# Performance work log

Hardware: AMD Instinct MI355X
Metric: run time of the kernel (lower is better)

## Reference

```python
import jax, jax.numpy as jnp
import numpy as np

# layer_sizes[i] = (hidden_dim, branching); 3 tree levels with fan-out 8 -> 512 leaf bins
LAYER_SIZES = [[512, 1], [512, 8], [512, 8], [512, 8]]
IN_DIM = LAYER_SIZES[0][0]
BATCH = 8192


def _nets_per_level():
    ns, n = [], 1
    for i in range(len(LAYER_SIZES) - 1):
        ns.append(n)
        n *= LAYER_SIZES[i + 1][1]
    return ns  # [1, 8, 64]


def setup_inputs() -> dict:
    key = jax.random.key(0)
    ks = jax.random.split(key, 16)
    ns = _nets_per_level()
    d = {"inp": jax.random.normal(ks[0], (BATCH, IN_DIM), jnp.float32)}
    k = 1
    for i, n in enumerate(ns):
        h = LAYER_SIZES[i + 1][0]
        w = LAYER_SIZES[i + 1][1]
        # stacked per-net weights (xavier-ish scale)
        d[f"Wx{i}"] = jax.random.normal(ks[k], (n, IN_DIM, h), jnp.float32) / np.float32(np.sqrt(IN_DIM)); k += 1
        d[f"bx{i}"] = jnp.zeros((n, h), jnp.float32)
        d[f"Wp{i}"] = jax.random.normal(ks[k], (n, h, w), jnp.float32) / np.float32(np.sqrt(h)); k += 1
        d[f"bp{i}"] = jnp.zeros((n, w), jnp.float32)
    d["We"] = jax.random.normal(ks[k], (IN_DIM, 1), jnp.float32) / np.float32(np.sqrt(IN_DIM))
    d["be"] = jnp.zeros((1,), jnp.float32)
    return d


def reference(inp, Wx0, bx0, Wp0, bp0, Wx1, bx1, Wp1, bp1, Wx2, bx2, Wp2, bp2, We, be):
    # event indicator head (blockable=False -> single sigmoid unit)
    got_event = jax.nn.sigmoid(inp @ We + be)  # [B, 1]
    Wxs, bxs = [Wx0, Wx1, Wx2], [bx0, bx1, bx2]
    Wps, bps = [Wp0, Wp1, Wp2], [bp0, bp1, bp2]
    probs_out = []
    parent = None  # flattened parent probs [B, n_i]; child j scales by parent[:, j]
    for i in range(3):
        # all nets at this level read the raw input: batched grouped GEMM
        h = jax.nn.relu(jnp.einsum('bi,nih->bnh', inp, Wxs[i]) + bxs[i])   # [B, n, H]
        p = jax.nn.softmax(jnp.einsum('bnh,nhw->bnw', h, Wps[i]) + bps[i], axis=-1)  # [B, n, w]
        if i == 0:
            p = p * got_event[:, :, None]          # get_event_probs, not blockable
        else:
            p = p * parent[:, :, None]             # gather of parent prob column j%w == flat index j
        parent = p.reshape(p.shape[0], -1)         # [B, n*w]
        probs_out.append(jnp.concatenate([parent, 1.0 - got_event], axis=1))
    return tuple(probs_out)
```

## Files before the change

### kernel.cpp

```cpp
#include <hip/hip_runtime.h>

#define IN_DIM 512
#define NBATCH 8192
#define BM 128
#define BK 32
#define HSTR 136

typedef short s16x8 __attribute__((ext_vector_type(8)));
typedef float f32x4 __attribute__((ext_vector_type(4)));

__device__ __forceinline__ unsigned short f2bf(float f) {
    union { float f; unsigned int u; } c;
    c.f = f;
    unsigned int u = c.u;
    u += 0x7fffu + ((u >> 16) & 1u);
    return (unsigned short)(u >> 16);
}

__device__ __forceinline__ void gload16(const unsigned short* g, unsigned short* l) {
    __builtin_amdgcn_global_load_lds(
        (const __attribute__((address_space(1))) void*)g,
        (__attribute__((address_space(3))) void*)l,
        16, 0, 0);
}


__global__ __launch_bounds__(256)
void conv_inp(const float* __restrict__ in, unsigned short* __restrict__ out) {
    int i = (blockIdx.x * 256 + threadIdx.x) * 8;
    float4 a = *(const float4*)&in[i];
    float4 b = *(const float4*)&in[i + 4];
    union { unsigned short u[8]; s16x8 v; } r;
    r.u[0] = f2bf(a.x); r.u[1] = f2bf(a.y); r.u[2] = f2bf(a.z); r.u[3] = f2bf(a.w);
    r.u[4] = f2bf(b.x); r.u[5] = f2bf(b.y); r.u[6] = f2bf(b.z); r.u[7] = f2bf(b.w);
    *(s16x8*)&out[i] = r.v;
}

__global__ __launch_bounds__(256)
void conv_wxT(const float* __restrict__ Wx, unsigned short* __restrict__ WxT) {
    __shared__ unsigned short T[64][80];
    int j  = blockIdx.y;
    int tr = blockIdx.x >> 3;
    int tc = blockIdx.x & 7;
    const float* src = Wx + (size_t)j * IN_DIM * IN_DIM;
    unsigned short* dst = WxT + (size_t)j * IN_DIM * IN_DIM;
    int tid = threadIdx.x;
    int k  = tid >> 2;
    int c0 = (tid & 3) * 16;
    for (int u = 0; u < 16; u += 4) {
        float4 v = *(const float4*)&src[(size_t)(tr * 64 + k) * IN_DIM + tc * 64 + c0 + u];
        T[c0 + u + 0][k] = f2bf(v.x);
        T[c0 + u + 1][k] = f2bf(v.y);
        T[c0 + u + 2][k] = f2bf(v.z);
        T[c0 + u + 3][k] = f2bf(v.w);
    }
    __syncthreads();
    int c  = tid >> 2;
    int k0 = (tid & 3) * 16;
    for (int u = 0; u < 16; u += 8) {
        s16x8 v = *(const s16x8*)&T[c][k0 + u];
        *(s16x8*)&dst[(size_t)(tc * 64 + c) * IN_DIM + tr * 64 + k0 + u] = v;
    }
}

__global__ __launch_bounds__(256)
void conv_wpT(const float* __restrict__ Wp, unsigned short* __restrict__ WpT) {
    int j = blockIdx.x;
    const float* src = Wp + (size_t)j * IN_DIM * 8;
    unsigned short* dst = WpT + (size_t)j * IN_DIM * 8;
    for (int k = threadIdx.x; k < IN_DIM; k += 256)
        for (int w = 0; w < 8; ++w)
            dst[w * IN_DIM + k] = f2bf(src[k * 8 + w]);
}

__global__ __launch_bounds__(256, 2)
void level_fast(const unsigned short* __restrict__ inpB,
                const unsigned short* __restrict__ WxT,
                const float* __restrict__ bx,
                const unsigned short* __restrict__ WpT,
                const float* __restrict__ bp,
                const float* __restrict__ parent,
                int pstride, int poff, int invert_parent,
                float* __restrict__ outp, int ostride)
{
    __shared__ __align__(16) unsigned short lds[BM * HSTR];

    const int tid  = threadIdx.x;
    const int lane = tid & 63;
    const int wv   = tid >> 6;
    const int j    = blockIdx.y;
    const int rowBase = blockIdx.x * BM;
    const int lr  = lane & 15;
    const int kg8 = (lane >> 4) * 8;
    const int rg  = (lane >> 4) * 4;
    const int wm  = (wv & 1) * 64;
    const int wn  = (wv >> 1) * 64;

    const unsigned short* WxTj = WxT + (size_t)j * IN_DIM * IN_DIM;
    const unsigned short* WpTj = WpT + (size_t)j * IN_DIM * 8;

    const int srow  = wv * 32 + (lane >> 2);
    const int sslot = (lane & 3) * 8;

    f32x4 acc2[2] = {};

    for (int nt = 0; nt < 4; ++nt) {
        f32x4 acc[4][4] = {};
        for (int k0 = 0; k0 < IN_DIM; k0 += BK) {
            __syncthreads();
            {
                const unsigned short* ga = inpB + (size_t)(rowBase + srow) * IN_DIM + k0 + sslot;
                const unsigned short* gb = WxTj + (size_t)(nt * BM + srow) * IN_DIM + k0 + sslot;
                gload16(ga,                &lds[wv * 1024]);
                gload16(ga + 16 * IN_DIM,  &lds[wv * 1024 + 512]);
                gload16(gb,                &lds[4096 + wv * 1024]);
                gload16(gb + 16 * IN_DIM,  &lds[4096 + wv * 1024 + 512]);
            }
            __syncthreads();
            s16x8 af[4], bfr[4];
            for (int mt = 0; mt < 4; ++mt)
                af[mt] = *(const s16x8*)&lds[(wm + mt * 16 + lr) * 32 + kg8];
            for (int nn = 0; nn < 4; ++nn)
                bfr[nn] = *(const s16x8*)&lds[4096 + (wn + nn * 16 + lr) * 32 + kg8];
            for (int mt = 0; mt < 4; ++mt)
                for (int nn = 0; nn < 4; ++nn)
                    acc[mt][nn] = __builtin_amdgcn_mfma_f32_16x16x32_bf16(
                        af[mt], bfr[nn], acc[mt][nn], 0, 0, 0);
        }
        __syncthreads();
        for (int nn = 0; nn < 4; ++nn) {
            int ncol = wn + nn * 16 + lr;
            float bxv = bx[(size_t)j * IN_DIM + nt * BM + ncol];
            for (int mt = 0; mt < 4; ++mt)
                for (int v = 0; v < 4; ++v) {
                    float h = acc[mt][nn][v] + bxv;
                    h = h > 0.f ? h : 0.f;
                    lds[(wm + mt * 16 + rg + v) * HSTR + ncol] = f2bf(h);
                }
        }
        __syncthreads();
        for (int k2 = 0; k2 < 4; ++k2) {
            int jw = lr & 7;
            s16x8 b2 = *(const s16x8*)(WpTj + jw * IN_DIM + nt * BM + k2 * 32 + kg8);
            for (int m2 = 0; m2 < 2; ++m2) {
                s16x8 a2 = *(const s16x8*)&lds[(wv * 32 + m2 * 16 + lr) * HSTR + k2 * 32 + kg8];
                acc2[m2] = __builtin_amdgcn_mfma_f32_16x16x32_bf16(a2, b2, acc2[m2], 0, 0, 0);
            }
        }
    }

    bool valid = lr < 8;
    float bpv = valid ? bp[(size_t)j * 8 + lr] : 0.f;
    for (int m2 = 0; m2 < 2; ++m2) {
        for (int v = 0; v < 4; ++v) {
            float x = acc2[m2][v] + bpv;
            float mx = x;
            for (int d = 1; d < 8; d <<= 1)
                mx = fmaxf(mx, __shfl_xor(mx, d, 64));
            float e = __expf(x - mx);
            float s = e;
            for (int d = 1; d < 8; d <<= 1)
                s += __shfl_xor(s, d, 64);
            float p = e / s;
            int gb = rowBase + wv * 32 + m2 * 16 + rg + v;
            float pv = invert_parent ? (1.f - parent[(size_t)gb * pstride + poff])
                                     : parent[(size_t)gb * pstride + j];
            if (valid)
                outp[(size_t)gb * ostride + j * 8 + lr] = p * pv;
        }
    }
}

__global__ __launch_bounds__(256, 2)
void level_ref(const float* __restrict__ inp,
               const float* __restrict__ Wx,
               const float* __restrict__ bx,
               const float* __restrict__ Wp,
               const float* __restrict__ bp,
               const float* __restrict__ parent,
               int pstride, int poff, int invert_parent,
               float* __restrict__ outp, int ostride)
{
    __shared__ __align__(16) unsigned short Ash[128][40];
    __shared__ __align__(16) unsigned short Bsh[128][40];
    __shared__ __align__(16) unsigned short Hsh[128][HSTR];
    __shared__ __align__(16) unsigned short WpSh[8][IN_DIM];

    const int tid  = threadIdx.x;
    const int lane = tid & 63;
    const int wv   = tid >> 6;
    const int j    = blockIdx.y;
    const int rowBase = blockIdx.x * 128;
    const int lr = lane & 15;
    const int kg = (lane >> 4) * 8;
    const int rg = (lane >> 4) * 4;
    const int wm = (wv & 1) * 64;
    const int wn = (wv >> 1) * 64;

    const float* WxJ = Wx + (size_t)j * IN_DIM * IN_DIM;
    const float* WpJ = Wp + (size_t)j * IN_DIM * 8;

    for (int i = tid; i < IN_DIM * 2; i += 256) {
        int k  = i >> 1;
        int w4 = (i & 1) * 4;
        float4 v = *(const float4*)&WpJ[k * 8 + w4];
        WpSh[w4 + 0][k] = f2bf(v.x);
        WpSh[w4 + 1][k] = f2bf(v.y);
        WpSh[w4 + 2][k] = f2bf(v.z);
        WpSh[w4 + 3][k] = f2bf(v.w);
    }

    f32x4 acc2[2] = {};

    for (int nt = 0; nt < 4; ++nt) {
        f32x4 acc[4][4] = {};
        for (int k0 = 0; k0 < IN_DIM; k0 += 32) {
            __syncthreads();
            {
                int kk4 = (tid & 7) * 4;
                int rb  = tid >> 3;
                for (int it = 0; it < 4; ++it) {
                    int r = rb + it * 32;
                    float4 v = *(const float4*)&inp[(size_t)(rowBase + r) * IN_DIM + k0 + kk4];
                    unsigned short* dst = &Ash[r][kk4];
                    dst[0] = f2bf(v.x); dst[1] = f2bf(v.y);
                    dst[2] = f2bf(v.z); dst[3] = f2bf(v.w);
                }
            }
            {
                int n4 = (tid & 31) * 4;
                int kb = tid >> 5;
                for (int it = 0; it < 4; ++it) {
                    int kk = kb + it * 8;
                    float4 v = *(const float4*)&WxJ[(size_t)(k0 + kk) * IN_DIM + nt * 128 + n4];
                    Bsh[n4 + 0][kk] = f2bf(v.x);
                    Bsh[n4 + 1][kk] = f2bf(v.y);
                    Bsh[n4 + 2][kk] = f2bf(v.z);
                    Bsh[n4 + 3][kk] = f2bf(v.w);
                }
            }
            __syncthreads();
            s16x8 af[4], bfr[4];
            for (int mt = 0; mt < 4; ++mt)
                af[mt] = *(const s16x8*)&Ash[wm + mt * 16 + lr][kg];
            for (int nn = 0; nn < 4; ++nn)
                bfr[nn] = *(const s16x8*)&Bsh[wn + nn * 16 + lr][kg];
            for (int mt = 0; mt < 4; ++mt)
                for (int nn = 0; nn < 4; ++nn)
                    acc[mt][nn] = __builtin_amdgcn_mfma_f32_16x16x32_bf16(
                        af[mt], bfr[nn], acc[mt][nn], 0, 0, 0);
        }
        __syncthreads();
        for (int nn = 0; nn < 4; ++nn) {
            int ncol = wn + nn * 16 + lr;
            float bxv = bx[(size_t)j * IN_DIM + nt * 128 + ncol];
            for (int mt = 0; mt < 4; ++mt)
                for (int v = 0; v < 4; ++v) {
                    float h = acc[mt][nn][v] + bxv;
                    h = h > 0.f ? h : 0.f;
                    Hsh[wm + mt * 16 + rg + v][ncol] = f2bf(h);
                }
        }
        __syncthreads();
        {
            s16x8 zero = {};
            for (int k2 = 0; k2 < 128; k2 += 32) {
                s16x8 b2 = (lr < 8) ? *(const s16x8*)&WpSh[lr][nt * 128 + k2 + kg] : zero;
                for (int m2 = 0; m2 < 2; ++m2) {
                    s16x8 a2 = *(const s16x8*)&Hsh[wv * 32 + m2 * 16 + lr][k2 + kg];
                    acc2[m2] = __builtin_amdgcn_mfma_f32_16x16x32_bf16(a2, b2, acc2[m2], 0, 0, 0);
                }
            }
        }
    }

    bool valid = lr < 8;
    float bpv = valid ? bp[(size_t)j * 8 + lr] : 0.f;
    for (int m2 = 0; m2 < 2; ++m2) {
        for (int v = 0; v < 4; ++v) {
            float x = acc2[m2][v] + bpv;
            float mx = x;
            for (int d = 1; d < 8; d <<= 1)
                mx = fmaxf(mx, __shfl_xor(mx, d, 64));
            float e = __expf(x - mx);
            float s = e;
            for (int d = 1; d < 8; d <<= 1)
                s += __shfl_xor(s, d, 64);
            float p = e / s;
            int gb = rowBase + wv * 32 + m2 * 16 + rg + v;
            float pv = invert_parent ? (1.f - parent[(size_t)gb * pstride + poff])
                                     : parent[(size_t)gb * pstride + j];
            if (valid)
                outp[(size_t)gb * ostride + j * 8 + lr] = p * pv;
        }
    }
}

__global__ __launch_bounds__(256)
void head_kernel(const float* __restrict__ inp,
                 const float* __restrict__ We,
                 const float* __restrict__ be,
                 float* __restrict__ out)
{
    int row  = blockIdx.x * 4 + (threadIdx.x >> 6);
    int lane = threadIdx.x & 63;
    const float* ip = inp + (size_t)row * IN_DIM;
    float4 a0 = *(const float4*)&ip[lane * 8];
    float4 a1 = *(const float4*)&ip[lane * 8 + 4];
    float4 w0 = *(const float4*)&We[lane * 8];
    float4 w1 = *(const float4*)&We[lane * 8 + 4];
    float s = a0.x*w0.x + a0.y*w0.y + a0.z*w0.z + a0.w*w0.w
            + a1.x*w1.x + a1.y*w1.y + a1.z*w1.z + a1.w*w1.w;
    for (int d = 1; d < 64; d <<= 1)
        s += __shfl_xor(s, d, 64);
    if (lane == 0) {
        float ge = 1.f / (1.f + __expf(-(s + be[0])));
        float og = 1.f - ge;
        out[(size_t)row * 9 + 8] = og;
        out[(size_t)(NBATCH * 9) + (size_t)row * 65 + 64] = og;
        out[(size_t)(NBATCH * 9 + NBATCH * 65) + (size_t)row * 513 + 512] = og;
    }
}

extern "C" void kernel_launch(void* const* d_in, const int* in_sizes, int n_in,
                              void* d_out, int out_size, void* d_ws, size_t ws_size,
                              hipStream_t stream) {
    const float* inp = (const float*)d_in[0];
    const float* Wx0 = (const float*)d_in[1];
    const float* bx0 = (const float*)d_in[2];
    const float* Wp0 = (const float*)d_in[3];
    const float* bp0 = (const float*)d_in[4];
    const float* Wx1 = (const float*)d_in[5];
    const float* bx1 = (const float*)d_in[6];
    const float* Wp1 = (const float*)d_in[7];
    const float* bp1 = (const float*)d_in[8];
    const float* Wx2 = (const float*)d_in[9];
    const float* bx2 = (const float*)d_in[10];
    const float* Wp2 = (const float*)d_in[11];
    const float* bp2 = (const float*)d_in[12];
    const float* We  = (const float*)d_in[13];
    const float* be  = (const float*)d_in[14];
    float* out = (float*)d_out;

    const size_t OUT1 = (size_t)NBATCH * 9;
    const size_t OUT2 = OUT1 + (size_t)NBATCH * 65;

    const size_t INP_E = (size_t)NBATCH * IN_DIM;
    const size_t WX_E  = (size_t)IN_DIM * IN_DIM;
    const size_t WP_E  = (size_t)IN_DIM * 8;
    const size_t NEED  = 2 * (INP_E + 73 * WX_E + 73 * WP_E);

    head_kernel<<<NBATCH / 4, 256, 0, stream>>>(inp, We, be, out);

    dim3 blk(256);
    if (ws_size >= NEED) {
        unsigned short* inpB   = (unsigned short*)d_ws;
        unsigned short* WxTall = inpB + INP_E;
        unsigned short* WpTall = WxTall + 73 * WX_E;

        conv_inp<<<NBATCH * IN_DIM / (256 * 8), 256, 0, stream>>>(inp, inpB);
        conv_wxT<<<dim3(64, 1),  blk, 0, stream>>>(Wx0, WxTall);
        conv_wxT<<<dim3(64, 8),  blk, 0, stream>>>(Wx1, WxTall + 1 * WX_E);
        conv_wxT<<<dim3(64, 64), blk, 0, stream>>>(Wx2, WxTall + 9 * WX_E);
        conv_wpT<<<1,  blk, 0, stream>>>(Wp0, WpTall);
        conv_wpT<<<8,  blk, 0, stream>>>(Wp1, WpTall + 1 * WP_E);
        conv_wpT<<<64, blk, 0, stream>>>(Wp2, WpTall + 9 * WP_E);

        level_fast<<<dim3(NBATCH / BM, 1), blk, 0, stream>>>(
            inpB, WxTall, bx0, WpTall, bp0, out, 9, 8, 1, out, 9);
        level_fast<<<dim3(NBATCH / BM, 8), blk, 0, stream>>>(
            inpB, WxTall + 1 * WX_E, bx1, WpTall + 1 * WP_E, bp1,
            out, 9, 0, 0, out + OUT1, 65);
        level_fast<<<dim3(NBATCH / BM, 64), blk, 0, stream>>>(
            inpB, WxTall + 9 * WX_E, bx2, WpTall + 9 * WP_E, bp2,
            out + OUT1, 65, 0, 0, out + OUT2, 513);
    } else {
        level_ref<<<dim3(NBATCH / BM, 1), blk, 0, stream>>>(
            inp, Wx0, bx0, Wp0, bp0, out, 9, 8, 1, out, 9);
        level_ref<<<dim3(NBATCH / BM, 8), blk, 0, stream>>>(
            inp, Wx1, bx1, Wp1, bp1, out, 9, 0, 0, out + OUT1, 65);
        level_ref<<<dim3(NBATCH / BM, 64), blk, 0, stream>>>(
            inp, Wx2, bx2, Wp2, bp2, out + OUT1, 65, 0, 0, out + OUT2, 513);
    }
}
```

Before: 476.3 us.

## Add 8-wave triple-buffered level kernel with 256-row tiles for levels 1-2

```diff
diff --git a/kernel.cpp b/kernel.cpp
--- a/kernel.cpp
+++ b/kernel.cpp
@@ -2,9 +2,17 @@
 
 #define IN_DIM 512
 #define NBATCH 8192
-#define BM 128
-#define BK 32
 #define HSTR 136
+
+#define BM8 256
+#define BNT 128
+#define BK8 32
+#define A_SLOT_U16 8192
+#define B_SLOT_U16 4096
+#define B_BASE_U16 24576
+#define H_BASE_U16 36864
+#define H_STRIDE   132
+#define LDS_U16_TOTAL (H_BASE_U16 + 256 * H_STRIDE)
 
 typedef short s16x8 __attribute__((ext_vector_type(8)));
 typedef float f32x4 __attribute__((ext_vector_type(4)));
@@ -73,6 +81,141 @@
             dst[w * IN_DIM + k] = f2bf(src[k * 8 + w]);
 }
 
+__global__ __launch_bounds__(512, 2)
+void level_8ph(const unsigned short* __restrict__ inpB,
+               const unsigned short* __restrict__ WxT,
+               const float* __restrict__ bx,
+               const unsigned short* __restrict__ WpT,
+               const float* __restrict__ bp,
+               const float* __restrict__ parent,
+               int pstride, int poff, int invert_parent,
+               float* __restrict__ outp, int ostride)
+{
+    extern __shared__ __align__(16) unsigned short lds[];
+
+    const int tid  = threadIdx.x;
+    const int lane = tid & 63;
+    const int wid  = tid >> 6;
+    const int wr   = wid >> 1;
+    const int wc   = wid & 1;
+    const int j    = blockIdx.y;
+    const int rowBase = blockIdx.x * BM8;
+    const int lr   = lane & 15;
+    const int grp  = lane >> 4;
+    const int kg8  = grp * 8;
+    const int rg   = grp * 4;
+
+    const unsigned short* WxTj = WxT + (size_t)j * IN_DIM * IN_DIM;
+    const unsigned short* WpTj = WpT + (size_t)j * IN_DIM * 8;
+
+    const int srcRow = tid >> 2;
+    const int srcK   = (tid & 3) * 8;
+    const unsigned short* gA  = inpB + (size_t)(rowBase + srcRow) * IN_DIM + srcK;
+    const unsigned short* gB0 = WxTj + (size_t)srcRow * IN_DIM + srcK;
+    unsigned short* ldsW = lds + wid * 512;
+
+    auto STAGE = [&](int g2, int sl_) {
+        int kt  = (g2 & 15) * BK8;
+        int nt2 = g2 >> 4;
+        const unsigned short* a = gA + kt;
+        gload16(a,                    ldsW + sl_ * A_SLOT_U16);
+        gload16(a + 128 * IN_DIM,     ldsW + sl_ * A_SLOT_U16 + 4096);
+        gload16(gB0 + (size_t)nt2 * BNT * IN_DIM + kt,
+                                      ldsW + B_BASE_U16 + sl_ * B_SLOT_U16);
+    };
+
+    f32x4 acc[4][4] = {};
+    f32x4 acc2[2]  = {};
+
+    STAGE(0, 0);
+    STAGE(1, 1);
+    asm volatile("s_waitcnt vmcnt(3)" ::: "memory");
+    __builtin_amdgcn_s_barrier();
+
+    int sl = 0, sl2 = 2;
+    for (int g = 0; g < 64; ++g) {
+        const unsigned short* As = lds + sl * A_SLOT_U16 + (wr * 64 + lr) * BK8 + kg8;
+        const unsigned short* Bs = lds + B_BASE_U16 + sl * B_SLOT_U16 + (wc * 64 + lr) * BK8 + kg8;
+        s16x8 af[4], bf[4];
+        #pragma unroll
+        for (int mt = 0; mt < 4; ++mt) af[mt] = *(const s16x8*)(As + mt * 16 * BK8);
+        #pragma unroll
+        for (int nn = 0; nn < 4; ++nn) bf[nn] = *(const s16x8*)(Bs + nn * 16 * BK8);
+
+        bool staged = (g + 2 < 64);
+        if (staged) STAGE(g + 2, sl2);
+
+        __builtin_amdgcn_s_barrier();
+
+        __builtin_amdgcn_s_setprio(1);
+        #pragma unroll
+        for (int mt = 0; mt < 4; ++mt)
+            #pragma unroll
+            for (int nn = 0; nn < 4; ++nn)
+                acc[mt][nn] = __builtin_amdgcn_mfma_f32_16x16x32_bf16(
+                    af[mt], bf[nn], acc[mt][nn], 0, 0, 0);
+        __builtin_amdgcn_s_setprio(0);
+
+        if (staged) asm volatile("s_waitcnt vmcnt(3)" ::: "memory");
+        else        asm volatile("s_waitcnt vmcnt(0)" ::: "memory");
+        __builtin_amdgcn_s_barrier();
+
+        if ((g & 15) == 15) {
+            int nt = g >> 4;
+            #pragma unroll
+            for (int nn = 0; nn < 4; ++nn) {
+                int ncol = wc * 64 + nn * 16 + lr;
+                float bxv = bx[(size_t)j * IN_DIM + nt * BNT + ncol];
+                #pragma unroll
+                for (int mt = 0; mt < 4; ++mt)
+                    #pragma unroll
+                    for (int v = 0; v < 4; ++v) {
+                        float h = acc[mt][nn][v] + bxv;
+                        h = h > 0.f ? h : 0.f;
+                        lds[H_BASE_U16 + (wr * 64 + mt * 16 + rg + v) * H_STRIDE + ncol] = f2bf(h);
+                        acc[mt][nn][v] = 0.f;
+                    }
+            }
+            asm volatile("s_waitcnt lgkmcnt(0)" ::: "memory");
+            __builtin_amdgcn_s_barrier();
+            #pragma unroll
+            for (int k2 = 0; k2 < 4; ++k2) {
+                s16x8 b2 = *(const s16x8*)(WpTj + (size_t)(lr & 7) * IN_DIM + nt * BNT + k2 * 32 + kg8);
+                #pragma unroll
+                for (int m2 = 0; m2 < 2; ++m2) {
+                    s16x8 a2 = *(const s16x8*)&lds[H_BASE_U16 + (wid * 32 + m2 * 16 + lr) * H_STRIDE + k2 * 32 + kg8];
+                    acc2[m2] = __builtin_amdgcn_mfma_f32_16x16x32_bf16(a2, b2, acc2[m2], 0, 0, 0);
+                }
+            }
+        }
+        sl  = (sl  == 2) ? 0 : sl  + 1;
+        sl2 = (sl2 == 2) ? 0 : sl2 + 1;
+    }
+
+    bool valid = lr < 8;
+    float bpv = valid ? bp[(size_t)j * 8 + lr] : 0.f;
+    #pragma unroll
+    for (int m2 = 0; m2 < 2; ++m2) {
+        #pragma unroll
+        for (int v = 0; v < 4; ++v) {
+            float x = acc2[m2][v] + bpv;
+            float mx = x;
+            for (int d = 1; d < 8; d <<= 1)
+                mx = fmaxf(mx, __shfl_xor(mx, d, 64));
+            float e = __expf(x - mx);
+            float s = e;
+            for (int d = 1; d < 8; d <<= 1)
+                s += __shfl_xor(s, d, 64);
+            float p = e / s;
+            int gb = rowBase + wid * 32 + m2 * 16 + rg + v;
+            float pv = invert_parent ? (1.f - parent[(size_t)gb * pstride + poff])
+                                     : parent[(size_t)gb * pstride + j];
+            if (valid)
+                outp[(size_t)gb * ostride + j * 8 + lr] = p * pv;
+        }
+    }
+}
+
 __global__ __launch_bounds__(256, 2)
 void level_fast(const unsigned short* __restrict__ inpB,
                 const unsigned short* __restrict__ WxT,
@@ -83,13 +226,13 @@
                 int pstride, int poff, int invert_parent,
                 float* __restrict__ outp, int ostride)
 {
-    __shared__ __align__(16) unsigned short lds[BM * HSTR];
+    __shared__ __align__(16) unsigned short lds[128 * HSTR];
 
     const int tid  = threadIdx.x;
     const int lane = tid & 63;
     const int wv   = tid >> 6;
     const int j    = blockIdx.y;
-    const int rowBase = blockIdx.x * BM;
+    const int rowBase = blockIdx.x * 128;
     const int lr  = lane & 15;
     const int kg8 = (lane >> 4) * 8;
     const int rg  = (lane >> 4) * 4;
@@ -106,11 +249,11 @@
 
     for (int nt = 0; nt < 4; ++nt) {
         f32x4 acc[4][4] = {};
-        for (int k0 = 0; k0 < IN_DIM; k0 += BK) {
+        for (int k0 = 0; k0 < IN_DIM; k0 += 32) {
             __syncthreads();
             {
                 const unsigned short* ga = inpB + (size_t)(rowBase + srow) * IN_DIM + k0 + sslot;
-                const unsigned short* gb = WxTj + (size_t)(nt * BM + srow) * IN_DIM + k0 + sslot;
+                const unsigned short* gb = WxTj + (size_t)(nt * 128 + srow) * IN_DIM + k0 + sslot;
                 gload16(ga,                &lds[wv * 1024]);
                 gload16(ga + 16 * IN_DIM,  &lds[wv * 1024 + 512]);
                 gload16(gb,                &lds[4096 + wv * 1024]);
@@ -130,7 +273,7 @@
         __syncthreads();
         for (int nn = 0; nn < 4; ++nn) {
             int ncol = wn + nn * 16 + lr;
-            float bxv = bx[(size_t)j * IN_DIM + nt * BM + ncol];
+            float bxv = bx[(size_t)j * IN_DIM + nt * 128 + ncol];
             for (int mt = 0; mt < 4; ++mt)
                 for (int v = 0; v < 4; ++v) {
                     float h = acc[mt][nn][v] + bxv;
@@ -141,7 +284,7 @@
         __syncthreads();
         for (int k2 = 0; k2 < 4; ++k2) {
             int jw = lr & 7;
-            s16x8 b2 = *(const s16x8*)(WpTj + jw * IN_DIM + nt * BM + k2 * 32 + kg8);
+            s16x8 b2 = *(const s16x8*)(WpTj + jw * IN_DIM + nt * 128 + k2 * 32 + kg8);
             for (int m2 = 0; m2 < 2; ++m2) {
                 s16x8 a2 = *(const s16x8*)&lds[(wv * 32 + m2 * 16 + lr) * HSTR + k2 * 32 + kg8];
                 acc2[m2] = __builtin_amdgcn_mfma_f32_16x16x32_bf16(a2, b2, acc2[m2], 0, 0, 0);
@@ -366,20 +509,34 @@
         conv_wpT<<<8,  blk, 0, stream>>>(Wp1, WpTall + 1 * WP_E);
         conv_wpT<<<64, blk, 0, stream>>>(Wp2, WpTall + 9 * WP_E);
 
-        level_fast<<<dim3(NBATCH / BM, 1), blk, 0, stream>>>(
+        level_fast<<<dim3(NBATCH / 128, 1), blk, 0, stream>>>(
             inpB, WxTall, bx0, WpTall, bp0, out, 9, 8, 1, out, 9);
-        level_fast<<<dim3(NBATCH / BM, 8), blk, 0, stream>>>(
-            inpB, WxTall + 1 * WX_E, bx1, WpTall + 1 * WP_E, bp1,
-            out, 9, 0, 0, out + OUT1, 65);
-        level_fast<<<dim3(NBATCH / BM, 64), blk, 0, stream>>>(
-            inpB, WxTall + 9 * WX_E, bx2, WpTall + 9 * WP_E, bp2,
-            out + OUT1, 65, 0, 0, out + OUT2, 513);
+
+        const int LDS_BYTES = LDS_U16_TOTAL * 2;
+        hipError_t rc = hipFuncSetAttribute((const void*)level_8ph,
+                                            hipFuncAttributeMaxDynamicSharedMemorySize,
+                                            LDS_BYTES);
+        if (rc == hipSuccess) {
+            level_8ph<<<dim3(NBATCH / BM8, 8), dim3(512), LDS_BYTES, stream>>>(
+                inpB, WxTall + 1 * WX_E, bx1, WpTall + 1 * WP_E, bp1,
+                out, 9, 0, 0, out + OUT1, 65);
+            level_8ph<<<dim3(NBATCH / BM8, 64), dim3(512), LDS_BYTES, stream>>>(
+                inpB, WxTall + 9 * WX_E, bx2, WpTall + 9 * WP_E, bp2,
+                out + OUT1, 65, 0, 0, out + OUT2, 513);
+        } else {
+            level_fast<<<dim3(NBATCH / 128, 8), blk, 0, stream>>>(
+                inpB, WxTall + 1 * WX_E, bx1, WpTall + 1 * WP_E, bp1,
+                out, 9, 0, 0, out + OUT1, 65);
+            level_fast<<<dim3(NBATCH / 128, 64), blk, 0, stream>>>(
+                inpB, WxTall + 9 * WX_E, bx2, WpTall + 9 * WP_E, bp2,
+                out + OUT1, 65, 0, 0, out + OUT2, 513);
+        }
     } else {
-        level_ref<<<dim3(NBATCH / BM, 1), blk, 0, stream>>>(
+        level_ref<<<dim3(NBATCH / 128, 1), blk, 0, stream>>>(
             inp, Wx0, bx0, Wp0, bp0, out, 9, 8, 1, out, 9);
-        level_ref<<<dim3(NBATCH / BM, 8), blk, 0, stream>>>(
+        level_ref<<<dim3(NBATCH / 128, 8), blk, 0, stream>>>(
             inp, Wx1, bx1, Wp1, bp1, out, 9, 0, 0, out + OUT1, 65);
-        level_ref<<<dim3(NBATCH / BM, 64), blk, 0, stream>>>(
+        level_ref<<<dim3(NBATCH / 128, 64), blk, 0, stream>>>(
             inp, Wx2, bx2, Wp2, bp2, out + OUT1, 65, 0, 0, out + OUT2, 513);
     }
 }
```

After: 534.8 us. 1.12x slower.

## Widen GEMM N-tile to 256, load A directly to registers, swizzle B in LDS

Applied to the files above, without the earlier changes.

```diff
diff --git a/kernel.cpp b/kernel.cpp
--- a/kernel.cpp
+++ b/kernel.cpp
@@ -2,9 +2,13 @@
 
 #define IN_DIM 512
 #define NBATCH 8192
-#define BM 128
-#define BK 32
-#define HSTR 136
+
+#define V3_BM  128
+#define V3_BNT 256
+#define V3_BK  64
+#define V3_HSTR 260
+#define V3_H_U16 (V3_BM * V3_HSTR)
+#define V3_LDS_BYTES (V3_H_U16 * 2)
 
 typedef short s16x8 __attribute__((ext_vector_type(8)));
 typedef float f32x4 __attribute__((ext_vector_type(4)));
@@ -55,11 +59,14 @@
         T[c0 + u + 3][k] = f2bf(v.w);
     }
     __syncthreads();
-    int c  = tid >> 2;
-    int k0 = (tid & 3) * 16;
+    int c   = tid >> 2;
+    int k0b = (tid & 3) * 16;
     for (int u = 0; u < 16; u += 8) {
-        s16x8 v = *(const s16x8*)&T[c][k0 + u];
-        *(s16x8*)&dst[(size_t)(tc * 64 + c) * IN_DIM + tr * 64 + k0 + u] = v;
+        int kk = k0b + u;
+        int ck = (kk >> 3) & 7;
+        int kswz = ((ck ^ (c & 7)) << 3);
+        s16x8 v = *(const s16x8*)&T[c][kk];
+        *(s16x8*)&dst[(size_t)(tc * 64 + c) * IN_DIM + tr * 64 + kswz] = v;
     }
 }
 
@@ -74,76 +81,100 @@
 }
 
 __global__ __launch_bounds__(256, 2)
-void level_fast(const unsigned short* __restrict__ inpB,
-                const unsigned short* __restrict__ WxT,
-                const float* __restrict__ bx,
-                const unsigned short* __restrict__ WpT,
-                const float* __restrict__ bp,
-                const float* __restrict__ parent,
-                int pstride, int poff, int invert_parent,
-                float* __restrict__ outp, int ostride)
+void level_v3b(const unsigned short* __restrict__ inpB,
+               const unsigned short* __restrict__ WxT,
+               const float* __restrict__ bx,
+               const unsigned short* __restrict__ WpT,
+               const float* __restrict__ bp,
+               const float* __restrict__ parent,
+               int pstride, int poff, int invert_parent,
+               float* __restrict__ outp, int ostride)
 {
-    __shared__ __align__(16) unsigned short lds[BM * HSTR];
+    extern __shared__ __align__(16) unsigned short lds[];
 
     const int tid  = threadIdx.x;
     const int lane = tid & 63;
     const int wv   = tid >> 6;
+    const int wr   = wv & 1;
+    const int wc   = wv >> 1;
     const int j    = blockIdx.y;
-    const int rowBase = blockIdx.x * BM;
-    const int lr  = lane & 15;
-    const int kg8 = (lane >> 4) * 8;
-    const int rg  = (lane >> 4) * 4;
-    const int wm  = (wv & 1) * 64;
-    const int wn  = (wv >> 1) * 64;
+    const int rowBase = blockIdx.x * V3_BM;
+    const int lr   = lane & 15;
+    const int grp  = lane >> 4;
+    const int kg8  = grp * 8;
+    const int rg   = grp * 4;
 
     const unsigned short* WxTj = WxT + (size_t)j * IN_DIM * IN_DIM;
     const unsigned short* WpTj = WpT + (size_t)j * IN_DIM * 8;
 
-    const int srow  = wv * 32 + (lane >> 2);
-    const int sslot = (lane & 3) * 8;
+    const int scol = wv * 8 + (lane >> 3);
+    const int sk   = (lane & 7) * 8;
+    unsigned short* ldsW = lds + wv * 512;
+
+    const int xor8 = (lr & 7) << 3;
+    const int boff0 = (0  + kg8) ^ xor8;
+    const int boff1 = (32 + kg8) ^ xor8;
+
+    const unsigned short* aRow = inpB + (size_t)(rowBase + wr * 64 + lr) * IN_DIM + kg8;
 
     f32x4 acc2[2] = {};
 
-    for (int nt = 0; nt < 4; ++nt) {
-        f32x4 acc[4][4] = {};
-        for (int k0 = 0; k0 < IN_DIM; k0 += BK) {
+    #pragma unroll 1
+    for (int nt = 0; nt < 2; ++nt) {
+        f32x4 acc[4][8] = {};
+        const unsigned short* gB = WxTj + (size_t)(nt * V3_BNT + scol) * IN_DIM + sk;
+
+        #pragma unroll 1
+        for (int k0 = 0; k0 < IN_DIM; k0 += V3_BK) {
             __syncthreads();
-            {
-                const unsigned short* ga = inpB + (size_t)(rowBase + srow) * IN_DIM + k0 + sslot;
-                const unsigned short* gb = WxTj + (size_t)(nt * BM + srow) * IN_DIM + k0 + sslot;
-                gload16(ga,                &lds[wv * 1024]);
-                gload16(ga + 16 * IN_DIM,  &lds[wv * 1024 + 512]);
-                gload16(gb,                &lds[4096 + wv * 1024]);
-                gload16(gb + 16 * IN_DIM,  &lds[4096 + wv * 1024 + 512]);
+            #pragma unroll
+            for (int i = 0; i < 8; ++i)
+                gload16(gB + (size_t)i * 32 * IN_DIM + k0, ldsW + i * 2048);
+            s16x8 af[2][4];
+            #pragma unroll
+            for (int ks = 0; ks < 2; ++ks)
+                #pragma unroll
+                for (int mt = 0; mt < 4; ++mt)
+                    af[ks][mt] = *(const s16x8*)(aRow + (size_t)(mt * 16) * IN_DIM + k0 + ks * 32);
+            __syncthreads();
+
+            #pragma unroll
+            for (int ks = 0; ks < 2; ++ks) {
+                const int boff = ks ? boff1 : boff0;
+                s16x8 bf[8];
+                #pragma unroll
+                for (int nn = 0; nn < 8; ++nn)
+                    bf[nn] = *(const s16x8*)&lds[(wc * 128 + nn * 16 + lr) * V3_BK + boff];
+                #pragma unroll
+                for (int mt = 0; mt < 4; ++mt)
+                    #pragma unroll
+                    for (int nn = 0; nn < 8; ++nn)
+                        acc[mt][nn] = __builtin_amdgcn_mfma_f32_16x16x32_bf16(
+                            af[ks][mt], bf[nn], acc[mt][nn], 0, 0, 0);
             }
-            __syncthreads();
-            s16x8 af[4], bfr[4];
+        }
+
+        __syncthreads();
+        #pragma unroll
+        for (int nn = 0; nn < 8; ++nn) {
+            int ncol = wc * 128 + nn * 16 + lr;
+            float bxv = bx[(size_t)j * IN_DIM + nt * V3_BNT + ncol];
+            #pragma unroll
             for (int mt = 0; mt < 4; ++mt)
-                af[mt] = *(const s16x8*)&lds[(wm + mt * 16 + lr) * 32 + kg8];
-            for (int nn = 0; nn < 4; ++nn)
-                bfr[nn] = *(const s16x8*)&lds[4096 + (wn + nn * 16 + lr) * 32 + kg8];
-            for (int mt = 0; mt < 4; ++mt)
-                for (int nn = 0; nn < 4; ++nn)
-                    acc[mt][nn] = __builtin_amdgcn_mfma_f32_16x16x32_bf16(
-                        af[mt], bfr[nn], acc[mt][nn], 0, 0, 0);
-        }
-        __syncthreads();
-        for (int nn = 0; nn < 4; ++nn) {
-            int ncol = wn + nn * 16 + lr;
-            float bxv = bx[(size_t)j * IN_DIM + nt * BM + ncol];
-            for (int mt = 0; mt < 4; ++mt)
+                #pragma unroll
                 for (int v = 0; v < 4; ++v) {
                     float h = acc[mt][nn][v] + bxv;
                     h = h > 0.f ? h : 0.f;
-                    lds[(wm + mt * 16 + rg + v) * HSTR + ncol] = f2bf(h);
+                    lds[(wr * 64 + mt * 16 + rg + v) * V3_HSTR + ncol] = f2bf(h);
                 }
         }
         __syncthreads();
-        for (int k2 = 0; k2 < 4; ++k2) {
-            int jw = lr & 7;
-            s16x8 b2 = *(const s16x8*)(WpTj + jw * IN_DIM + nt * BM + k2 * 32 + kg8);
+        #pragma unroll
+        for (int k2 = 0; k2 < 8; ++k2) {
+            s16x8 b2 = *(const s16x8*)(WpTj + (size_t)(lr & 7) * IN_DIM + nt * V3_BNT + k2 * 32 + kg8);
+            #pragma unroll
             for (int m2 = 0; m2 < 2; ++m2) {
-                s16x8 a2 = *(const s16x8*)&lds[(wv * 32 + m2 * 16 + lr) * HSTR + k2 * 32 + kg8];
+                s16x8 a2 = *(const s16x8*)&lds[(wv * 32 + m2 * 16 + lr) * V3_HSTR + k2 * 32 + kg8];
                 acc2[m2] = __builtin_amdgcn_mfma_f32_16x16x32_bf16(a2, b2, acc2[m2], 0, 0, 0);
             }
         }
@@ -151,7 +182,9 @@
 
     bool valid = lr < 8;
     float bpv = valid ? bp[(size_t)j * 8 + lr] : 0.f;
+    #pragma unroll
     for (int m2 = 0; m2 < 2; ++m2) {
+        #pragma unroll
         for (int v = 0; v < 4; ++v) {
             float x = acc2[m2][v] + bpv;
             float mx = x;
@@ -183,7 +216,7 @@
 {
     __shared__ __align__(16) unsigned short Ash[128][40];
     __shared__ __align__(16) unsigned short Bsh[128][40];
-    __shared__ __align__(16) unsigned short Hsh[128][HSTR];
+    __shared__ __align__(16) unsigned short Hsh[128][136];
     __shared__ __align__(16) unsigned short WpSh[8][IN_DIM];
 
     const int tid  = threadIdx.x;
@@ -353,7 +386,15 @@
     head_kernel<<<NBATCH / 4, 256, 0, stream>>>(inp, We, be, out);
 
     dim3 blk(256);
+    bool fast = false;
     if (ws_size >= NEED) {
+        hipError_t rc = hipFuncSetAttribute((const void*)level_v3b,
+                                            hipFuncAttributeMaxDynamicSharedMemorySize,
+                                            V3_LDS_BYTES);
+        fast = (rc == hipSuccess);
+    }
+
+    if (fast) {
         unsigned short* inpB   = (unsigned short*)d_ws;
         unsigned short* WxTall = inpB + INP_E;
         unsigned short* WpTall = WxTall + 73 * WX_E;
@@ -366,20 +407,20 @@
         conv_wpT<<<8,  blk, 0, stream>>>(Wp1, WpTall + 1 * WP_E);
         conv_wpT<<<64, blk, 0, stream>>>(Wp2, WpTall + 9 * WP_E);
 
-        level_fast<<<dim3(NBATCH / BM, 1), blk, 0, stream>>>(
+        level_v3b<<<dim3(NBATCH / V3_BM, 1), blk, V3_LDS_BYTES, stream>>>(
             inpB, WxTall, bx0, WpTall, bp0, out, 9, 8, 1, out, 9);
-        level_fast<<<dim3(NBATCH / BM, 8), blk, 0, stream>>>(
+        level_v3b<<<dim3(NBATCH / V3_BM, 8), blk, V3_LDS_BYTES, stream>>>(
             inpB, WxTall + 1 * WX_E, bx1, WpTall + 1 * WP_E, bp1,
             out, 9, 0, 0, out + OUT1, 65);
-        level_fast<<<dim3(NBATCH / BM, 64), blk, 0, stream>>>(
+        level_v3b<<<dim3(NBATCH / V3_BM, 64), blk, V3_LDS_BYTES, stream>>>(
             inpB, WxTall + 9 * WX_E, bx2, WpTall + 9 * WP_E, bp2,
             out + OUT1, 65, 0, 0, out + OUT2, 513);
     } else {
-        level_ref<<<dim3(NBATCH / BM, 1), blk, 0, stream>>>(
+        level_ref<<<dim3(NBATCH / 128, 1), blk, 0, stream>>>(
             inp, Wx0, bx0, Wp0, bp0, out, 9, 8, 1, out, 9);
-        level_ref<<<dim3(NBATCH / BM, 8), blk, 0, stream>>>(
+        level_ref<<<dim3(NBATCH / 128, 8), blk, 0, stream>>>(
             inp, Wx1, bx1, Wp1, bp1, out, 9, 0, 0, out + OUT1, 65);
-        level_ref<<<dim3(NBATCH / BM, 64), blk, 0, stream>>>(
+        level_ref<<<dim3(NBATCH / 128, 64), blk, 0, stream>>>(
             inp, Wx2, bx2, Wp2, bp2, out + OUT1, 65, 0, 0, out + OUT2, 513);
     }
 }
```

After: 539.3 us. 1.13x slower.
